# Optimization experiments

Measured on AMD Instinct MI355X. Metric: run time of the kernel, lower is better.

Reference implementation:

```python
import jax, jax.numpy as jnp
import numpy as np


def _minplus(x, W):
    # x: [B, in], W: [out, in] -> y[b,i] = min_j (x[b,j] + W[i,j])
    return jnp.min(x[:, None, :] + W[None, :, :], axis=-1)


def _maxbplus(x, W, b):
    # x: [B, in], W: [out, in], b: [out] -> y[b,i] = max_j (x[b,j] + W[i,j]) + b[i]
    return jnp.max(x[:, None, :] + W[None, :, :], axis=-1) + b


def _basic_block(x, w1, w2, b2, sw1=None, sw2=None, sb2=None):
    out = _maxbplus(_minplus(x, w1), w2, b2)
    sc = x if sw1 is None else _maxbplus(_minplus(x, sw1), sw2, sb2)
    return jnp.minimum(out, sc)


def setup_inputs() -> dict:
    key = jax.random.key(0)
    B, IN, OUT = 1024, 256, 512
    ks = jax.random.split(key, 16)
    s = 0.05
    inp = {
        'x': jax.random.normal(ks[0], (B, IN), jnp.float32),
        # layers 1-3: in==out==IN, no block shortcut params
        'l1_w1': jax.random.normal(ks[1], (IN, IN), jnp.float32) * s,
        'l1_w2': jax.random.normal(ks[2], (IN, IN), jnp.float32) * s,
        'l1_b2': jax.random.normal(ks[3], (IN,), jnp.float32) * s,
        'l2_w1': jax.random.normal(ks[4], (IN, IN), jnp.float32) * s,
        'l2_w2': jax.random.normal(ks[5], (IN, IN), jnp.float32) * s,
        'l2_b2': jax.random.normal(ks[6], (IN,), jnp.float32) * s,
        'l3_w1': jax.random.normal(ks[7], (IN, IN), jnp.float32) * s,
        'l3_w2': jax.random.normal(ks[8], (IN, IN), jnp.float32) * s,
        'l3_b2': jax.random.normal(ks[9], (IN,), jnp.float32) * s,
        # layer 4: IN -> OUT, has block-level shortcut
        'l4_w1': jax.random.normal(ks[10], (OUT, IN), jnp.float32) * s,
        'l4_w2': jax.random.normal(ks[11], (OUT, OUT), jnp.float32) * s,
        'l4_b2': jax.random.normal(ks[12], (OUT,), jnp.float32) * s,
        'l4_sw1': jax.random.normal(ks[13], (OUT, IN), jnp.float32) * s,
        'l4_sw2': jax.random.normal(ks[14], (OUT, OUT), jnp.float32) * s,
        'l4_sb2': jax.random.normal(ks[15], (OUT,), jnp.float32) * s,
    }
    k2 = jax.random.split(jax.random.fold_in(key, 1), 3)
    inp['sc_w1'] = jax.random.normal(k2[0], (OUT, IN), jnp.float32) * s
    inp['sc_w2'] = jax.random.normal(k2[1], (OUT, OUT), jnp.float32) * s
    inp['sc_b2'] = jax.random.normal(k2[2], (OUT,), jnp.float32) * s
    return inp


def reference(x, l1_w1, l1_w2, l1_b2, l2_w1, l2_w2, l2_b2,
              l3_w1, l3_w2, l3_b2, l4_w1, l4_w2, l4_b2,
              l4_sw1, l4_sw2, l4_sb2, sc_w1, sc_w2, sc_b2):
    out = _basic_block(x, l1_w1, l1_w2, l1_b2)            # layer1 (IN->IN)
    out = _basic_block(out, l2_w1, l2_w2, l2_b2)          # layer2
    out = _basic_block(out, l3_w1, l3_w2, l3_b2)          # layer3
    out = _basic_block(out, l4_w1, l4_w2, l4_b2,
                       l4_sw1, l4_sw2, l4_sb2)            # layer4 (IN->OUT)
    sc = _maxbplus(_minplus(x, sc_w1), sc_w2, sc_b2)      # bottleneck shortcut
    return jnp.maximum(out, sc)
```

## Files before the change

### kernel.cpp

```cpp
#include <hip/hip_runtime.h>
#include <math.h>


typedef _Float16 h2 __attribute__((ext_vector_type(2)));
typedef _Float16 h8 __attribute__((ext_vector_type(8)));

template<int M> __device__ __forceinline__ h2 rdv(h2 a, h2 b) {
    if constexpr (M) return __builtin_elementwise_max(a, b);
    else             return __builtin_elementwise_min(a, b);
}

struct NetP {
    const float* x;
    const h8 *w11, *w12, *w21, *w22, *w31, *w32;
    const h8 *w41, *w42, *sw1, *sw2, *scw1, *scw2;
    const _Float16 *b12, *b22, *b32, *b42, *sb2, *scb2;
    float* out;
};

template<int ISMAX, int R, int K, bool GOUT>
__device__ __forceinline__ void stage(
    const h8* __restrict__ Wc,
    const _Float16* __restrict__ bias,
    const _Float16* __restrict__ X,
    const _Float16* __restrict__ E1,
    const _Float16* __restrict__ E2,
    _Float16* __restrict__ Y,
    float* __restrict__ gout, int b0,
    h2* __restrict__ part)
{
    constexpr int NRG = R / 2;
    constexpr int KS  = 1024 / NRG;
    static_assert(NRG * KS == 1024, "thread mapping");
    const int tid  = threadIdx.x;
    const int rowg = tid & (NRG - 1);
    const int kq   = tid / NRG;
    const int r0 = rowg, r1 = rowg + NRG;
    constexpr int NC = (K / 8) / KS;
    const int kc0 = kq * NC;

    const h2* Xh2 = (const h2*)X;

    h2 a0, a1;
    {
        h8 w0 = Wc[(size_t)kc0 * R + r0];
        h8 w1 = Wc[(size_t)kc0 * R + r1];
        const h2* xk = Xh2 + kc0 * 8;
        h2 xs = xk[0];
        h2 u = {w0[0], w0[0]}, v = {w1[0], w1[0]};
        a0 = xs + u; a1 = xs + v;
#pragma unroll
        for (int j = 1; j < 8; ++j) {
            xs = xk[j];
            h2 uu = {w0[j], w0[j]}, vv = {w1[j], w1[j]};
            a0 = rdv<ISMAX>(a0, xs + uu);
            a1 = rdv<ISMAX>(a1, xs + vv);
        }
    }
#pragma unroll 2
    for (int kc = kc0 + 1; kc < kc0 + NC; ++kc) {
        h8 w0 = Wc[(size_t)kc * R + r0];
        h8 w1 = Wc[(size_t)kc * R + r1];
        const h2* xk = Xh2 + kc * 8;
#pragma unroll
        for (int j = 0; j < 8; ++j) {
            h2 xs = xk[j];
            h2 uu = {w0[j], w0[j]}, vv = {w1[j], w1[j]};
            a0 = rdv<ISMAX>(a0, xs + uu);
            a1 = rdv<ISMAX>(a1, xs + vv);
        }
    }

    if (kq) {
        h2* pp = part + (size_t)(kq - 1) * R;
        pp[r0] = a0; pp[r1] = a1;
    }
    __syncthreads();
    if (kq == 0) {
#pragma unroll
        for (int qq = 0; qq < KS - 1; ++qq) {
            const h2* pp = part + (size_t)qq * R;
            a0 = rdv<ISMAX>(a0, pp[r0]);
            a1 = rdv<ISMAX>(a1, pp[r1]);
        }
        if (ISMAX) {
            _Float16 q0 = bias[r0], q1 = bias[r1];
            h2 s0 = {q0, q0}, s1 = {q1, q1};
            a0 += s0; a1 += s1;
        }
        if (E1) {
            const h2* e = (const h2*)E1;
            a0 = __builtin_elementwise_min(a0, e[r0]);
            a1 = __builtin_elementwise_min(a1, e[r1]);
        }
        if (E2) {
            const h2* e = (const h2*)E2;
            a0 = __builtin_elementwise_max(a0, e[r0]);
            a1 = __builtin_elementwise_max(a1, e[r1]);
        }
        if constexpr (GOUT) {
            gout[(size_t)(b0 + 0) * 512 + r0] = (float)a0[0];
            gout[(size_t)(b0 + 1) * 512 + r0] = (float)a0[1];
            gout[(size_t)(b0 + 0) * 512 + r1] = (float)a1[0];
            gout[(size_t)(b0 + 1) * 512 + r1] = (float)a1[1];
        } else {
            h2* y = (h2*)Y;
            y[r0] = a0; y[r1] = a1;
        }
    }
    __syncthreads();
}

__global__ __launch_bounds__(1024) void netf(NetP p)
{
    __shared__ __align__(16) _Float16 X0[256 * 2];
    __shared__ __align__(16) _Float16 B0[512 * 2], B1[512 * 2];
    __shared__ __align__(16) _Float16 B2[512 * 2], B3[512 * 2];
    __shared__ __align__(16) h2 part[1792];
    const int tid = threadIdx.x;
    const int b0  = blockIdx.x * 2;

    if (tid < 512) {
        const int bl = tid >> 8;
        const int k  = tid & 255;
        X0[k * 2 + bl] = (_Float16)p.x[(size_t)(b0 + bl) * 256 + k];
    }
    __syncthreads();

    float* o = p.out;
    stage<0,512,256,false>(p.scw1, nullptr, X0, nullptr, nullptr, B0, o, b0, part);
    stage<1,512,512,false>(p.scw2, p.scb2,  B0, nullptr, nullptr, B1, o, b0, part);
    stage<0,256,256,false>(p.w11, nullptr, X0, nullptr, nullptr, B0, o, b0, part);
    stage<1,256,256,false>(p.w12, p.b12,   B0, X0,      nullptr, B2, o, b0, part);
    stage<0,256,256,false>(p.w21, nullptr, B2, nullptr, nullptr, B0, o, b0, part);
    stage<1,256,256,false>(p.w22, p.b22,   B0, B2,      nullptr, B3, o, b0, part);
    stage<0,256,256,false>(p.w31, nullptr, B3, nullptr, nullptr, B0, o, b0, part);
    stage<1,256,256,false>(p.w32, p.b32,   B0, B3,      nullptr, B2, o, b0, part);
    stage<0,512,256,false>(p.w41, nullptr, B2, nullptr, nullptr, B0, o, b0, part);
    stage<0,512,256,false>(p.sw1, nullptr, B2, nullptr, nullptr, B3, o, b0, part);
    stage<1,512,512,false>(p.w42, p.b42,   B0, nullptr, nullptr, B2, o, b0, part);
    stage<1,512,512,true >(p.sw2, p.sb2,   B3, B2,      B1, nullptr, o, b0, part);
}

struct Prep {
    const float* s[12]; h8* d[12]; int R[12]; int K[12];
    const float* bs[6]; _Float16* bd[6]; int bn[6];
};
__global__ __launch_bounds__(256) void cvtw(Prep p)
{
    const int m = blockIdx.y;
    if (m == 12) {
        if (blockIdx.x != 0) return;
        for (int s = 0; s < 6; ++s)
            for (int i = threadIdx.x; i < p.bn[s]; i += 256)
                p.bd[s][i] = (_Float16)p.bs[s][i];
        return;
    }
    const int R = p.R[m], K = p.K[m];
    const int tilesR = R >> 6;
    const int nt = tilesR * (K >> 6);
    const int t = blockIdx.x;
    if (t >= nt) return;
    const int tr = t % tilesR, tk = t / tilesR;

    __shared__ float s[64][65];
    const int lane = threadIdx.x & 63, ty = threadIdx.x >> 6;
    const float* src = p.s[m];
#pragma unroll
    for (int r = ty; r < 64; r += 4)
        s[r][lane] = src[(size_t)(tr * 64 + r) * K + tk * 64 + lane];
    __syncthreads();
    h8* dst = p.d[m];
#pragma unroll
    for (int c = 0; c < 2; ++c) {
        int cc = ty + c * 4;
        h8 v;
#pragma unroll
        for (int j = 0; j < 8; ++j) v[j] = (_Float16)s[lane][cc * 8 + j];
        dst[(size_t)(tk * 8 + cc) * R + tr * 64 + lane] = v;
    }
}

extern "C" void kernel_launch(void* const* d_in, const int* in_sizes, int n_in,
                              void* d_out, int out_size, void* d_ws, size_t ws_size,
                              hipStream_t stream) {
    (void)in_sizes; (void)n_in; (void)ws_size; (void)out_size;
    const float* fin[19];
    for (int i = 0; i < 19; ++i) fin[i] = (const float*)d_in[i];

    _Float16* hw = (_Float16*)d_ws;

    _Float16* w11c  = hw;
    _Float16* w12c  = hw + 65536;
    _Float16* w21c  = hw + 131072;
    _Float16* w22c  = hw + 196608;
    _Float16* w31c  = hw + 262144;
    _Float16* w32c  = hw + 327680;
    _Float16* w41c  = hw + 393216;
    _Float16* w42c  = hw + 524288;
    _Float16* sw1c  = hw + 786432;
    _Float16* sw2c  = hw + 917504;
    _Float16* scw1c = hw + 1179648;
    _Float16* scw2c = hw + 1310720;
    _Float16* bia   = hw + 1572864;
    _Float16* b12 = bia, *b22 = bia + 256, *b32 = bia + 512;
    _Float16* b42 = bia + 768, *sb2 = bia + 1280, *scb2 = bia + 1792;

    Prep cw;
    const float* wsrc[12] = {fin[1], fin[2], fin[4], fin[5], fin[7], fin[8],
                             fin[10], fin[11], fin[13], fin[14], fin[16], fin[17]};
    _Float16* wdst[12]    = {w11c, w12c, w21c, w22c, w31c, w32c,
                             w41c, w42c, sw1c, sw2c, scw1c, scw2c};
    const int wR[12] = {256,256,256,256,256,256, 512,512,512,512,512,512};
    const int wK[12] = {256,256,256,256,256,256, 256,512,256,512,256,512};
    for (int i = 0; i < 12; ++i) {
        cw.s[i] = wsrc[i]; cw.d[i] = (h8*)wdst[i]; cw.R[i] = wR[i]; cw.K[i] = wK[i];
    }
    const float* bsrc[6] = {fin[3], fin[6], fin[9], fin[12], fin[15], fin[18]};
    _Float16* bdst[6]    = {b12, b22, b32, b42, sb2, scb2};
    const int bn[6]      = {256, 256, 256, 512, 512, 512};
    for (int i = 0; i < 6; ++i) { cw.bs[i] = bsrc[i]; cw.bd[i] = bdst[i]; cw.bn[i] = bn[i]; }

    NetP p;
    p.x   = fin[0];
    p.w11 = (const h8*)w11c; p.w12 = (const h8*)w12c;
    p.w21 = (const h8*)w21c; p.w22 = (const h8*)w22c;
    p.w31 = (const h8*)w31c; p.w32 = (const h8*)w32c;
    p.w41 = (const h8*)w41c; p.w42 = (const h8*)w42c;
    p.sw1 = (const h8*)sw1c; p.sw2 = (const h8*)sw2c;
    p.scw1 = (const h8*)scw1c; p.scw2 = (const h8*)scw2c;
    p.b12 = b12; p.b22 = b22; p.b32 = b32; p.b42 = b42; p.sb2 = sb2; p.scb2 = scb2;
    p.out = (float*)d_out;

    cvtw<<<dim3(64, 13), 256, 0, stream>>>(cw);
    netf<<<dim3(512), dim3(1024), 0, stream>>>(p);
}
```

Before: 78.63 us.

## Switch to per-batch activation layout with 4 rows per thread, halve block size

Activations move from interleaved batch-pair storage to separate rows, so each thread loads eight k values of x as one h8 vector per batch. Each thread now computes four output rows, each packed as an h2 over consecutive k pairs, and reduces the pair only at the end. This raises register-level reuse of x and W and cuts per-element scalar broadcasts. Blocks shrink from 1024 to 512 threads, so there is less parallelism for hiding latency, and the epilogue becomes scalar.

Measured after the change: 82.46 us. 1.05x slower.

```diff
diff --git a/kernel.cpp b/kernel.cpp
--- a/kernel.cpp
+++ b/kernel.cpp
@@ -5,10 +5,15 @@
 typedef _Float16 h2 __attribute__((ext_vector_type(2)));
 typedef _Float16 h8 __attribute__((ext_vector_type(8)));
 
-template<int M> __device__ __forceinline__ h2 rdv(h2 a, h2 b) {
+template<int M, typename V> __device__ __forceinline__ V rdv(V a, V b) {
     if constexpr (M) return __builtin_elementwise_max(a, b);
     else             return __builtin_elementwise_min(a, b);
 }
+template<int M> __device__ __forceinline__ _Float16 rd1(_Float16 a, _Float16 b) {
+    if constexpr (M) return a > b ? a : b;
+    else             return a < b ? a : b;
+}
+#define XS(v, I0, I1) __builtin_shufflevector(v, v, I0, I1)
 
 struct NetP {
     const float* x;
@@ -27,103 +32,102 @@
     const _Float16* __restrict__ E2,
     _Float16* __restrict__ Y,
     float* __restrict__ gout, int b0,
-    h2* __restrict__ part)
+    _Float16* __restrict__ part)
 {
-    constexpr int NRG = R / 2;
-    constexpr int KS  = 1024 / NRG;
-    static_assert(NRG * KS == 1024, "thread mapping");
+    constexpr int NRG = R / 4;
+    constexpr int KS  = 512 / NRG;
+    constexpr int NC  = (K / 8) / KS;
+    static_assert(NRG * KS == 512, "thread mapping");
     const int tid  = threadIdx.x;
     const int rowg = tid & (NRG - 1);
     const int kq   = tid / NRG;
-    const int r0 = rowg, r1 = rowg + NRG;
-    constexpr int NC = (K / 8) / KS;
-    const int kc0 = kq * NC;
-
-    const h2* Xh2 = (const h2*)X;
-
-    h2 a0, a1;
+    const int kc0  = kq * NC;
+
+    const h8* Xc0 = (const h8*)X + kc0;
+    const h8* Xc1 = (const h8*)(X + K) + kc0;
+
+    h2 a00, a01, a10, a11, a20, a21, a30, a31;
+
+#define RDA(a, b) rdv<ISMAX>((a), (b))
+#define PIECE(J0, J1)                                                   \
+    {   h2 xa_ = XS(xa, J0, J1), xb_ = XS(xb, J0, J1); h2 t;            \
+        t = XS(w0, J0, J1); a00 = RDA(a00, xa_ + t); a01 = RDA(a01, xb_ + t); \
+        t = XS(w1, J0, J1); a10 = RDA(a10, xa_ + t); a11 = RDA(a11, xb_ + t); \
+        t = XS(w2, J0, J1); a20 = RDA(a20, xa_ + t); a21 = RDA(a21, xb_ + t); \
+        t = XS(w3, J0, J1); a30 = RDA(a30, xa_ + t); a31 = RDA(a31, xb_ + t); }
+
     {
-        h8 w0 = Wc[(size_t)kc0 * R + r0];
-        h8 w1 = Wc[(size_t)kc0 * R + r1];
-        const h2* xk = Xh2 + kc0 * 8;
-        h2 xs = xk[0];
-        h2 u = {w0[0], w0[0]}, v = {w1[0], w1[0]};
-        a0 = xs + u; a1 = xs + v;
-#pragma unroll
-        for (int j = 1; j < 8; ++j) {
-            xs = xk[j];
-            h2 uu = {w0[j], w0[j]}, vv = {w1[j], w1[j]};
-            a0 = rdv<ISMAX>(a0, xs + uu);
-            a1 = rdv<ISMAX>(a1, xs + vv);
+        h8 xa = Xc0[0], xb = Xc1[0];
+        const h8* Wr = Wc + (size_t)kc0 * R + rowg;
+        h8 w0 = Wr[0], w1 = Wr[NRG], w2 = Wr[2 * NRG], w3 = Wr[3 * NRG];
+        {   h2 xa_ = XS(xa, 0, 1), xb_ = XS(xb, 0, 1); h2 t;
+            t = XS(w0, 0, 1); a00 = xa_ + t; a01 = xb_ + t;
+            t = XS(w1, 0, 1); a10 = xa_ + t; a11 = xb_ + t;
+            t = XS(w2, 0, 1); a20 = xa_ + t; a21 = xb_ + t;
+            t = XS(w3, 0, 1); a30 = xa_ + t; a31 = xb_ + t;
         }
+        PIECE(2, 3) PIECE(4, 5) PIECE(6, 7)
     }
 #pragma unroll 2
-    for (int kc = kc0 + 1; kc < kc0 + NC; ++kc) {
-        h8 w0 = Wc[(size_t)kc * R + r0];
-        h8 w1 = Wc[(size_t)kc * R + r1];
-        const h2* xk = Xh2 + kc * 8;
-#pragma unroll
-        for (int j = 0; j < 8; ++j) {
-            h2 xs = xk[j];
-            h2 uu = {w0[j], w0[j]}, vv = {w1[j], w1[j]};
-            a0 = rdv<ISMAX>(a0, xs + uu);
-            a1 = rdv<ISMAX>(a1, xs + vv);
+    for (int kc = 1; kc < NC; ++kc) {
+        h8 xa = Xc0[kc], xb = Xc1[kc];
+        const h8* Wr = Wc + (size_t)(kc0 + kc) * R + rowg;
+        h8 w0 = Wr[0], w1 = Wr[NRG], w2 = Wr[2 * NRG], w3 = Wr[3 * NRG];
+        PIECE(0, 1) PIECE(2, 3) PIECE(4, 5) PIECE(6, 7)
+    }
+#undef PIECE
+
+    h8 v8;
+    v8[0] = rd1<ISMAX>(a00[0], a00[1]); v8[1] = rd1<ISMAX>(a01[0], a01[1]);
+    v8[2] = rd1<ISMAX>(a10[0], a10[1]); v8[3] = rd1<ISMAX>(a11[0], a11[1]);
+    v8[4] = rd1<ISMAX>(a20[0], a20[1]); v8[5] = rd1<ISMAX>(a21[0], a21[1]);
+    v8[6] = rd1<ISMAX>(a30[0], a30[1]); v8[7] = rd1<ISMAX>(a31[0], a31[1]);
+
+    if (kq) *(h8*)(part + ((size_t)(kq - 1) * NRG + rowg) * 8) = v8;
+    __syncthreads();
+    if (kq == 0) {
+#pragma unroll
+        for (int qq = 0; qq < KS - 1; ++qq)
+            v8 = rdv<ISMAX>(v8, *(const h8*)(part + ((size_t)qq * NRG + rowg) * 8));
+
+#pragma unroll
+        for (int i = 0; i < 4; ++i) {
+            const int r = rowg + i * NRG;
+            _Float16 oc0 = v8[2 * i], oc1 = v8[2 * i + 1];
+            if (ISMAX) { _Float16 bi = bias[r]; oc0 += bi; oc1 += bi; }
+            if (E1) {
+                _Float16 e0 = E1[r], e1 = E1[R + r];
+                oc0 = oc0 < e0 ? oc0 : e0; oc1 = oc1 < e1 ? oc1 : e1;
+            }
+            if (E2) {
+                _Float16 e0 = E2[r], e1 = E2[R + r];
+                oc0 = oc0 > e0 ? oc0 : e0; oc1 = oc1 > e1 ? oc1 : e1;
+            }
+            if constexpr (GOUT) {
+                gout[(size_t)(b0 + 0) * 512 + r] = (float)oc0;
+                gout[(size_t)(b0 + 1) * 512 + r] = (float)oc1;
+            } else {
+                Y[r] = oc0; Y[R + r] = oc1;
+            }
         }
     }
-
-    if (kq) {
-        h2* pp = part + (size_t)(kq - 1) * R;
-        pp[r0] = a0; pp[r1] = a1;
-    }
-    __syncthreads();
-    if (kq == 0) {
-#pragma unroll
-        for (int qq = 0; qq < KS - 1; ++qq) {
-            const h2* pp = part + (size_t)qq * R;
-            a0 = rdv<ISMAX>(a0, pp[r0]);
-            a1 = rdv<ISMAX>(a1, pp[r1]);
-        }
-        if (ISMAX) {
-            _Float16 q0 = bias[r0], q1 = bias[r1];
-            h2 s0 = {q0, q0}, s1 = {q1, q1};
-            a0 += s0; a1 += s1;
-        }
-        if (E1) {
-            const h2* e = (const h2*)E1;
-            a0 = __builtin_elementwise_min(a0, e[r0]);
-            a1 = __builtin_elementwise_min(a1, e[r1]);
-        }
-        if (E2) {
-            const h2* e = (const h2*)E2;
-            a0 = __builtin_elementwise_max(a0, e[r0]);
-            a1 = __builtin_elementwise_max(a1, e[r1]);
-        }
-        if constexpr (GOUT) {
-            gout[(size_t)(b0 + 0) * 512 + r0] = (float)a0[0];
-            gout[(size_t)(b0 + 1) * 512 + r0] = (float)a0[1];
-            gout[(size_t)(b0 + 0) * 512 + r1] = (float)a1[0];
-            gout[(size_t)(b0 + 1) * 512 + r1] = (float)a1[1];
-        } else {
-            h2* y = (h2*)Y;
-            y[r0] = a0; y[r1] = a1;
-        }
-    }
-    __syncthreads();
-}
-
-__global__ __launch_bounds__(1024) void netf(NetP p)
+#undef RDA
+    __syncthreads();
+}
+
+__global__ __launch_bounds__(512) void netf(NetP p)
 {
-    __shared__ __align__(16) _Float16 X0[256 * 2];
-    __shared__ __align__(16) _Float16 B0[512 * 2], B1[512 * 2];
-    __shared__ __align__(16) _Float16 B2[512 * 2], B3[512 * 2];
-    __shared__ __align__(16) h2 part[1792];
+    __shared__ __align__(16) _Float16 X0[2 * 256];
+    __shared__ __align__(16) _Float16 B0[2 * 512], B1[2 * 512];
+    __shared__ __align__(16) _Float16 B2[2 * 512], B3[2 * 512];
+    __shared__ __align__(16) _Float16 part[3584];
     const int tid = threadIdx.x;
     const int b0  = blockIdx.x * 2;
 
-    if (tid < 512) {
+    {
         const int bl = tid >> 8;
         const int k  = tid & 255;
-        X0[k * 2 + bl] = (_Float16)p.x[(size_t)(b0 + bl) * 256 + k];
+        X0[bl * 256 + k] = (_Float16)p.x[(size_t)(b0 + bl) * 256 + k];
     }
     __syncthreads();
 
@@ -233,5 +237,5 @@
     p.out = (float*)d_out;
 
     cvtw<<<dim3(64, 13), 256, 0, stream>>>(cw);
-    netf<<<dim3(512), dim3(1024), 0, stream>>>(p);
-}
+    netf<<<dim3(512), dim3(512), 0, stream>>>(p);
+}
```
